# Kernel optimization log

Hardware: AMD Instinct MI355X
Metric: run time of the kernel (lower is better)

Reference implementation:

```python
import jax, jax.numpy as jnp
import numpy as np

EMBEDDING_DIM = 32  # hard-coded in the original module
HEAD_SIZE = 2048
B, T = 8, 2048  # T must be <= HEAD_SIZE (tril buffer is head_size x head_size)


def setup_inputs() -> dict:
    key = jax.random.key(0)
    kx, kk, kq, kv = jax.random.split(key, 4)
    x = jax.random.normal(kx, (B, T, EMBEDDING_DIM), dtype=jnp.float32)
    # torch nn.Linear(EMBEDDING_DIM, head_size, bias=False) computes x @ W.T with
    # W of shape [head_size, EMBEDDING_DIM]; we store the transposed [in, out] form.
    scale = (1.0 / np.sqrt(EMBEDDING_DIM)).astype(np.float32)
    Wk = jax.random.normal(kk, (EMBEDDING_DIM, HEAD_SIZE), dtype=jnp.float32) * scale
    Wq = jax.random.normal(kq, (EMBEDDING_DIM, HEAD_SIZE), dtype=jnp.float32) * scale
    Wv = jax.random.normal(kv, (EMBEDDING_DIM, HEAD_SIZE), dtype=jnp.float32) * scale
    return {"x": x, "Wk": Wk, "Wq": Wq, "Wv": Wv}


def reference(x, Wk, Wq, Wv):
    b, t, c = x.shape  # c == EMBEDDING_DIM
    k = x @ Wk  # [b, t, head_size]
    q = x @ Wq  # [b, t, head_size]
    v = x @ Wv  # [b, t, head_size]
    # NB: original scales by c**-0.5 where c is the *input* embedding dim (32).
    scores = jnp.einsum('bth,bsh->bts', q, k) * (c ** -0.5)  # [b, t, t]
    causal = jnp.tril(jnp.ones((t, t), dtype=bool))
    scores = jnp.where(causal, scores, -jnp.inf)
    attn = jax.nn.softmax(scores, axis=-1)
    return attn @ v  # [b, t, head_size]
```

## Files before the change

### kernel.cpp

```cpp
#include <hip/hip_runtime.h>

#define BB 8
#define TT 2048
#define CC 32
#define HH 2048
#define QB 128
#define HB 128
#define SCALE 0.17677669529663687f
#define K2E   0.25503255741f

typedef _Float16 f16;
typedef f16 f16x8 __attribute__((ext_vector_type(8)));
typedef f16 f16x4 __attribute__((ext_vector_type(4)));
typedef float f32x4 __attribute__((ext_vector_type(4)));

__global__ __launch_bounds__(256) void mk_kernel(const float* __restrict__ Wq,
                                                 const float* __restrict__ Wk,
                                                 float* __restrict__ M) {
    const int o = blockIdx.x * 4 + (threadIdx.x >> 6);
    const int lane = threadIdx.x & 63;
    const int c = o >> 5, cp = o & 31;
    const float4* a = (const float4*)(Wq + (size_t)c * HH);
    const float4* b = (const float4*)(Wk + (size_t)cp * HH);
    float acc = 0.f;
    #pragma unroll
    for (int i = 0; i < 8; i++) {
        float4 av = a[lane + i * 64], bv = b[lane + i * 64];
        acc += av.x * bv.x + av.y * bv.y + av.z * bv.z + av.w * bv.w;
    }
    #pragma unroll
    for (int off = 1; off < 64; off <<= 1) acc += __shfl_xor(acc, off, 64);
    if (lane == 0) M[c * 32 + cp] = acc;
}

__global__ __launch_bounds__(256) void proj2_kernel(const float* __restrict__ x,
                                                    const float* __restrict__ M,
                                                    f16* __restrict__ yh,
                                                    f16* __restrict__ xh) {
    __shared__ float xs2[32][33];
    const int tid = threadIdx.x;
    const size_t rbase = (size_t)blockIdx.x * 32;
    const int r = tid >> 3, c4 = (tid & 7) * 4;
    float4 xv = *(const float4*)&x[(rbase + r) * CC + c4];
    xs2[r][c4 + 0] = xv.x; xs2[r][c4 + 1] = xv.y;
    xs2[r][c4 + 2] = xv.z; xs2[r][c4 + 3] = xv.w;
    f16x4 xf = {(f16)xv.x, (f16)xv.y, (f16)xv.z, (f16)xv.w};
    *(f16x4*)&xh[(rbase + r) * CC + c4] = xf;
    __syncthreads();
    float a0 = 0.f, a1 = 0.f, a2 = 0.f, a3 = 0.f;
    #pragma unroll
    for (int c = 0; c < 32; c++) {
        const float xr = xs2[r][c];
        const float4 mv = *(const float4*)&M[c * 32 + c4];
        a0 += xr * mv.x; a1 += xr * mv.y; a2 += xr * mv.z; a3 += xr * mv.w;
    }
    f16x4 yf = {(f16)a0, (f16)a1, (f16)a2, (f16)a3};
    *(f16x4*)&yh[(rbase + r) * CC + c4] = yf;
}

__global__ __launch_bounds__(256, 3) void attn_kernel(
    const f16* __restrict__ xh, const f16* __restrict__ yh,
    const float* __restrict__ Wv, float* __restrict__ out)
{
    const int bid = blockIdx.x;
    const int qt  = 15 - (bid >> 7);
    const int b   = (bid >> 4) & 7;
    const int ht  = bid & 15;
    const int tid = threadIdx.x;
    const int lane = tid & 63, wave = tid >> 6;
    const int g = lane >> 4, li = lane & 15;
    const int wr = wave >> 1, wc = wave & 1;
    const int qbase = qt * QB, hbase = ht * HB;
    const int qrow0 = qbase + wr * 64;
    const int nst = 2 * qt + 2;

    __shared__ __align__(16) f16 smem[64 * 40 + 128 * 72 + 128 * 72];
    f16 (*xs)[40] = (f16(*)[40])smem;
    f16 (*vt)[72] = (f16(*)[72])(smem + 64 * 40);
    f16 (*ps)[72] = (f16(*)[72])(smem + 64 * 40 + 128 * 72);
    __shared__ float mh[2][128];
    __shared__ float lh[2][128];

    const f16* xp = xh + (size_t)b * TT * CC;
    const f16* yp = yh + (size_t)b * TT * CC;

    f16x8 af[4];
    #pragma unroll
    for (int rf = 0; rf < 4; rf++)
        af[rf] = *(const f16x8*)&yp[(size_t)(qbase + wr * 64 + rf * 16 + li) * CC + g * 8];

    f16x8 wv[4];
    #pragma unroll
    for (int hf = 0; hf < 4; hf++) {
        #pragma unroll
        for (int j = 0; j < 8; j++)
            wv[hf][j] = (f16)Wv[(size_t)(g * 8 + j) * HH + hbase + wc * 64 + hf * 16 + li];
    }

    const int rr = tid >> 2, c8 = (tid & 3) * 8;

    float mp[4] = {-3e38f, -3e38f, -3e38f, -3e38f};
    f16 (*x4)[64][40] = (f16(*)[64][40])smem;
    for (int ch = 0; ch * 4 < nst; ch++) {
        __syncthreads();
        #pragma unroll
        for (int j = 0; j < 4; j++) {
            const int st = ch * 4 + j;
            if (st < nst)
                *(f16x8*)&x4[j][rr][c8] = *(const f16x8*)&xp[(size_t)(st * 64 + rr) * CC + c8];
        }
        __syncthreads();
        #pragma unroll
        for (int j = 0; j < 4; j++) {
            const int st = ch * 4 + j;
            if (st < nst) {
                const int sbase = st * 64;
                const bool diag = (sbase + 63) > qrow0;
                #pragma unroll
                for (int sfi = 0; sfi < 2; sfi++) {
                    const f16x8 xa = *(const f16x8*)&x4[j][(2 * wc + sfi) * 16 + li][g * 8];
                    const int sb2 = sbase + (2 * wc + sfi) * 16 + g * 4;
                    #pragma unroll
                    for (int rf = 0; rf < 4; rf++) {
                        f32x4 z = {};
                        f32x4 sc = __builtin_amdgcn_mfma_f32_16x16x32_f16(xa, af[rf], z, 0, 0, 0);
                        const int qg = qbase + wr * 64 + rf * 16 + li;
                        #pragma unroll
                        for (int reg = 0; reg < 4; reg++) {
                            float v = sc[reg];
                            if (diag && (sb2 + reg) > qg) v = -3e38f;
                            mp[rf] = fmaxf(mp[rf], v);
                        }
                    }
                }
            }
        }
    }
    #pragma unroll
    for (int rf = 0; rf < 4; rf++) {
        mp[rf] = fmaxf(mp[rf], __shfl_xor(mp[rf], 16, 64));
        mp[rf] = fmaxf(mp[rf], __shfl_xor(mp[rf], 32, 64));
    }
    if (g == 0) {
        #pragma unroll
        for (int rf = 0; rf < 4; rf++) mh[wc][wr * 64 + rf * 16 + li] = mp[rf];
    }
    __syncthreads();
    float m2[4];
    #pragma unroll
    for (int rf = 0; rf < 4; rf++)
        m2[rf] = fmaxf(mh[0][wr * 64 + rf * 16 + li], mh[1][wr * 64 + rf * 16 + li]) * K2E;

    f16x8 xn = *(const f16x8*)&xp[(size_t)rr * CC + c8];
    *(f16x8*)&xs[rr][c8] = xn;
    __syncthreads();

    f32x4 o[4][4] = {};
    float lp[4] = {0.f, 0.f, 0.f, 0.f};
    f16x4 pf0[4], pf1[4];
    f16x4 vf0[4], vf1[4];

    for (int st = 0; st <= nst; st++) {
        const int sbase = st * 64;
        const bool haveQ = (st < nst);
        if (haveQ) {
            if (st + 1 < nst)
                xn = *(const f16x8*)&xp[(size_t)((st + 1) * 64 + rr) * CC + c8];
            const bool diag = (sbase + 63) > qrow0;
            const f16x8 xa0 = *(const f16x8*)&xs[(2 * wc + 0) * 16 + li][g * 8];
            const f16x8 xa1 = *(const f16x8*)&xs[(2 * wc + 1) * 16 + li][g * 8];
            const f16x8 xw0 = *(const f16x8*)&xs[(2 * wr + 0) * 16 + li][g * 8];
            const f16x8 xw1 = *(const f16x8*)&xs[(2 * wr + 1) * 16 + li][g * 8];
            #pragma unroll
            for (int sfi = 0; sfi < 2; sfi++) {
                const f16x8 xa = sfi ? xa1 : xa0;
                const int sb2 = sbase + (2 * wc + sfi) * 16 + g * 4;
                #pragma unroll
                for (int rf = 0; rf < 4; rf++) {
                    f32x4 z = {};
                    f32x4 sc = __builtin_amdgcn_mfma_f32_16x16x32_f16(xa, af[rf], z, 0, 0, 0);
                    const int qg = qbase + wr * 64 + rf * 16 + li;
                    f16x4 pv;
                    #pragma unroll
                    for (int reg = 0; reg < 4; reg++) {
                        float e = exp2f(fmaf(sc[reg], K2E, -m2[rf]));
                        if (diag && (sb2 + reg) > qg) e = 0.f;
                        lp[rf] += e;
                        pv[reg] = (f16)e;
                    }
                    if (sfi == 0) pf0[rf] = pv; else pf1[rf] = pv;
                }
            }
            #pragma unroll
            for (int sfw = 0; sfw < 2; sfw++) {
                const f16x8 xw = sfw ? xw1 : xw0;
                #pragma unroll
                for (int hf = 0; hf < 4; hf++) {
                    f32x4 z = {};
                    f32x4 vc = __builtin_amdgcn_mfma_f32_16x16x32_f16(xw, wv[hf], z, 0, 0, 0);
                    f16x4 vv4;
                    #pragma unroll
                    for (int reg = 0; reg < 4; reg++) vv4[reg] = (f16)vc[reg];
                    if (sfw == 0) vf0[hf] = vv4; else vf1[hf] = vv4;
                }
            }
        }
        if (st > 0) {
            #pragma unroll
            for (int kk = 0; kk < 2; kk++) {
                f16x8 pa[4];
                #pragma unroll
                for (int rf = 0; rf < 4; rf++) {
                    const int prow = wr * 64 + rf * 16 + li;
                    pa[rf] = *(const f16x8*)&ps[prow][(kk * 32 + g * 8) ^ (((prow >> 2) & 3) << 4)];
                }
                #pragma unroll
                for (int hf = 0; hf < 4; hf++) {
                    const int vrow = wc * 64 + hf * 16 + li;
                    const f16x8 vb = *(const f16x8*)&vt[vrow][(kk * 32 + g * 8) ^ (((vrow >> 3) & 3) << 4)];
                    #pragma unroll
                    for (int rf = 0; rf < 4; rf++)
                        o[rf][hf] = __builtin_amdgcn_mfma_f32_16x16x32_f16(pa[rf], vb, o[rf][hf], 0, 0, 0);
                }
            }
        }
        __syncthreads();
        if (haveQ) {
            #pragma unroll
            for (int rf = 0; rf < 4; rf++) {
                const int prow = wr * 64 + rf * 16 + li;
                const int swp = ((prow >> 2) & 3) << 4;
                *(f16x4*)&ps[prow][((2 * wc + 0) * 16 + g * 4) ^ swp] = pf0[rf];
                *(f16x4*)&ps[prow][((2 * wc + 1) * 16 + g * 4) ^ swp] = pf1[rf];
            }
            #pragma unroll
            for (int hf = 0; hf < 4; hf++) {
                const int vrow = wc * 64 + hf * 16 + li;
                const int swv = ((vrow >> 3) & 3) << 4;
                *(f16x4*)&vt[vrow][((2 * wr + 0) * 16 + g * 4) ^ swv] = vf0[hf];
                *(f16x4*)&vt[vrow][((2 * wr + 1) * 16 + g * 4) ^ swv] = vf1[hf];
            }
            if (st + 1 < nst)
                *(f16x8*)&xs[rr][c8] = xn;
            __syncthreads();
        }
    }

    #pragma unroll
    for (int rf = 0; rf < 4; rf++) {
        lp[rf] += __shfl_xor(lp[rf], 16, 64);
        lp[rf] += __shfl_xor(lp[rf], 32, 64);
    }
    if (g == 0) {
        #pragma unroll
        for (int rf = 0; rf < 4; rf++) lh[wc][wr * 64 + rf * 16 + li] = lp[rf];
    }
    __syncthreads();
    float* op = out + (size_t)b * TT * HH;
    #pragma unroll
    for (int rf = 0; rf < 4; rf++) {
        #pragma unroll
        for (int reg = 0; reg < 4; reg++) {
            const int ql = wr * 64 + rf * 16 + g * 4 + reg;
            const float inv = 1.f / (lh[0][ql] + lh[1][ql]);
            #pragma unroll
            for (int hf = 0; hf < 4; hf++)
                op[(size_t)(qbase + ql) * HH + hbase + wc * 64 + hf * 16 + li] = o[rf][hf][reg] * inv;
        }
    }
}

extern "C" void kernel_launch(void* const* d_in, const int* in_sizes, int n_in,
                              void* d_out, int out_size, void* d_ws, size_t ws_size,
                              hipStream_t stream) {
    const float* x  = (const float*)d_in[0];
    const float* Wk = (const float*)d_in[1];
    const float* Wq = (const float*)d_in[2];
    const float* Wv = (const float*)d_in[3];
    float* out = (float*)d_out;

    float* Mp = (float*)d_ws;
    f16* xh = (f16*)((char*)d_ws + 4096);
    f16* yh = xh + (size_t)BB * TT * CC;

    mk_kernel<<<256, 256, 0, stream>>>(Wq, Wk, Mp);
    proj2_kernel<<<(BB * TT) / 32, 256, 0, stream>>>(x, Mp, yh, xh);
    attn_kernel<<<BB * (TT / QB) * (HH / HB), 256, 0, stream>>>(xh, yh, Wv, out);
}
```

Baseline: 484.1 us.

## Precompute softmax row max and sum in a separate kernel shared across head tiles

The per-row softmax max and normalizer are now computed once per (batch, query tile) in a new ml_kernel and written to workspace. Before, each of the 16 head-tile blocks recomputed the max pass redundantly. The attention kernel now loads these stats instead of running its own max pass and sum accumulation. This removes duplicated QK score work, at the cost of an extra launch and a small serial kernel with only 128 blocks of uneven causal work.

```diff
diff --git a/kernel.cpp b/kernel.cpp
--- a/kernel.cpp
+++ b/kernel.cpp
@@ -6,7 +6,6 @@
 #define HH 2048
 #define QB 128
 #define HB 128
-#define SCALE 0.17677669529663687f
 #define K2E   0.25503255741f
 
 typedef _Float16 f16;
@@ -58,9 +57,142 @@
     *(f16x4*)&yh[(rbase + r) * CC + c4] = yf;
 }
 
+__global__ __launch_bounds__(256) void ml_kernel(const f16* __restrict__ xh,
+                                                 const f16* __restrict__ yh,
+                                                 float* __restrict__ m2g,
+                                                 float* __restrict__ lig) {
+    const int b = blockIdx.x >> 4, qt = blockIdx.x & 15;
+    const int tid = threadIdx.x;
+    const int lane = tid & 63, wave = tid >> 6;
+    const int g = lane >> 4, li = lane & 15;
+    const int wr = wave >> 1, wc = wave & 1;
+    const int qbase = qt * QB;
+    const int qrow0 = qbase + wr * 64;
+    const int nst = 2 * qt + 2;
+
+    __shared__ __align__(16) f16 x4[4][64][40];
+    __shared__ float mh[2][128];
+    __shared__ float lh[2][128];
+
+    const f16* xp = xh + (size_t)b * TT * CC;
+    const f16* yp = yh + (size_t)b * TT * CC;
+
+    f16x8 af[4];
+    #pragma unroll
+    for (int rf = 0; rf < 4; rf++)
+        af[rf] = *(const f16x8*)&yp[(size_t)(qbase + wr * 64 + rf * 16 + li) * CC + g * 8];
+
+    const int rr = tid >> 2, c8 = (tid & 3) * 8;
+
+    float mp[4] = {-3e38f, -3e38f, -3e38f, -3e38f};
+    for (int ch = 0; ch * 4 < nst; ch++) {
+        __syncthreads();
+        #pragma unroll
+        for (int j = 0; j < 4; j++) {
+            const int st = ch * 4 + j;
+            if (st < nst)
+                *(f16x8*)&x4[j][rr][c8] = *(const f16x8*)&xp[(size_t)(st * 64 + rr) * CC + c8];
+        }
+        __syncthreads();
+        #pragma unroll
+        for (int j = 0; j < 4; j++) {
+            const int st = ch * 4 + j;
+            if (st < nst) {
+                const int sbase = st * 64;
+                const bool diag = (sbase + 63) > qrow0;
+                #pragma unroll
+                for (int sfi = 0; sfi < 2; sfi++) {
+                    const f16x8 xa = *(const f16x8*)&x4[j][(2 * wc + sfi) * 16 + li][g * 8];
+                    const int sb2 = sbase + (2 * wc + sfi) * 16 + g * 4;
+                    #pragma unroll
+                    for (int rf = 0; rf < 4; rf++) {
+                        f32x4 z = {};
+                        f32x4 sc = __builtin_amdgcn_mfma_f32_16x16x32_f16(xa, af[rf], z, 0, 0, 0);
+                        const int qg = qbase + wr * 64 + rf * 16 + li;
+                        #pragma unroll
+                        for (int reg = 0; reg < 4; reg++) {
+                            float v = sc[reg];
+                            if (diag && (sb2 + reg) > qg) v = -3e38f;
+                            mp[rf] = fmaxf(mp[rf], v);
+                        }
+                    }
+                }
+            }
+        }
+    }
+    #pragma unroll
+    for (int rf = 0; rf < 4; rf++) {
+        mp[rf] = fmaxf(mp[rf], __shfl_xor(mp[rf], 16, 64));
+        mp[rf] = fmaxf(mp[rf], __shfl_xor(mp[rf], 32, 64));
+    }
+    if (g == 0) {
+        #pragma unroll
+        for (int rf = 0; rf < 4; rf++) mh[wc][wr * 64 + rf * 16 + li] = mp[rf];
+    }
+    __syncthreads();
+    float m2[4];
+    #pragma unroll
+    for (int rf = 0; rf < 4; rf++)
+        m2[rf] = fmaxf(mh[0][wr * 64 + rf * 16 + li], mh[1][wr * 64 + rf * 16 + li]) * K2E;
+
+    float lp[4] = {0.f, 0.f, 0.f, 0.f};
+    for (int ch = 0; ch * 4 < nst; ch++) {
+        __syncthreads();
+        #pragma unroll
+        for (int j = 0; j < 4; j++) {
+            const int st = ch * 4 + j;
+            if (st < nst)
+                *(f16x8*)&x4[j][rr][c8] = *(const f16x8*)&xp[(size_t)(st * 64 + rr) * CC + c8];
+        }
+        __syncthreads();
+        #pragma unroll
+        for (int j = 0; j < 4; j++) {
+            const int st = ch * 4 + j;
+            if (st < nst) {
+                const int sbase = st * 64;
+                const bool diag = (sbase + 63) > qrow0;
+                #pragma unroll
+                for (int sfi = 0; sfi < 2; sfi++) {
+                    const f16x8 xa = *(const f16x8*)&x4[j][(2 * wc + sfi) * 16 + li][g * 8];
+                    const int sb2 = sbase + (2 * wc + sfi) * 16 + g * 4;
+                    #pragma unroll
+                    for (int rf = 0; rf < 4; rf++) {
+                        f32x4 z = {};
+                        f32x4 sc = __builtin_amdgcn_mfma_f32_16x16x32_f16(xa, af[rf], z, 0, 0, 0);
+                        const int qg = qbase + wr * 64 + rf * 16 + li;
+                        #pragma unroll
+                        for (int reg = 0; reg < 4; reg++) {
+                            float e = exp2f(fmaf(sc[reg], K2E, -m2[rf]));
+                            if (diag && (sb2 + reg) > qg) e = 0.f;
+                            lp[rf] += e;
+                        }
+                    }
+                }
+            }
+        }
+    }
+    #pragma unroll
+    for (int rf = 0; rf < 4; rf++) {
+        lp[rf] += __shfl_xor(lp[rf], 16, 64);
+        lp[rf] += __shfl_xor(lp[rf], 32, 64);
+    }
+    if (g == 0) {
+        #pragma unroll
+        for (int rf = 0; rf < 4; rf++) lh[wc][wr * 64 + rf * 16 + li] = lp[rf];
+    }
+    __syncthreads();
+    if (tid < 128) {
+        const float mv = fmaxf(mh[0][tid], mh[1][tid]) * K2E;
+        const float lv = lh[0][tid] + lh[1][tid];
+        m2g[(size_t)b * TT + qbase + tid] = mv;
+        lig[(size_t)b * TT + qbase + tid] = 1.f / lv;
+    }
+}
+
 __global__ __launch_bounds__(256, 3) void attn_kernel(
     const f16* __restrict__ xh, const f16* __restrict__ yh,
-    const float* __restrict__ Wv, float* __restrict__ out)
+    const float* __restrict__ Wv, const float* __restrict__ m2g,
+    const float* __restrict__ lig, float* __restrict__ out)
 {
     const int bid = blockIdx.x;
     const int qt  = 15 - (bid >> 7);
@@ -78,12 +210,17 @@
     f16 (*xs)[40] = (f16(*)[40])smem;
     f16 (*vt)[72] = (f16(*)[72])(smem + 64 * 40);
     f16 (*ps)[72] = (f16(*)[72])(smem + 64 * 40 + 128 * 72);
-    __shared__ float mh[2][128];
-    __shared__ float lh[2][128];
+    __shared__ float mrow[128];
+    __shared__ float lrow[128];
 
     const f16* xp = xh + (size_t)b * TT * CC;
     const f16* yp = yh + (size_t)b * TT * CC;
 
+    if (tid < 128) {
+        mrow[tid] = m2g[(size_t)b * TT + qbase + tid];
+        lrow[tid] = lig[(size_t)b * TT + qbase + tid];
+    }
+
     f16x8 af[4];
     #pragma unroll
     for (int rf = 0; rf < 4; rf++)
@@ -98,65 +235,16 @@
     }
 
     const int rr = tid >> 2, c8 = (tid & 3) * 8;
-
-    float mp[4] = {-3e38f, -3e38f, -3e38f, -3e38f};
-    f16 (*x4)[64][40] = (f16(*)[64][40])smem;
-    for (int ch = 0; ch * 4 < nst; ch++) {
-        __syncthreads();
-        #pragma unroll
-        for (int j = 0; j < 4; j++) {
-            const int st = ch * 4 + j;
-            if (st < nst)
-                *(f16x8*)&x4[j][rr][c8] = *(const f16x8*)&xp[(size_t)(st * 64 + rr) * CC + c8];
-        }
-        __syncthreads();
-        #pragma unroll
-        for (int j = 0; j < 4; j++) {
-            const int st = ch * 4 + j;
-            if (st < nst) {
-                const int sbase = st * 64;
-                const bool diag = (sbase + 63) > qrow0;
-                #pragma unroll
-                for (int sfi = 0; sfi < 2; sfi++) {
-                    const f16x8 xa = *(const f16x8*)&x4[j][(2 * wc + sfi) * 16 + li][g * 8];
-                    const int sb2 = sbase + (2 * wc + sfi) * 16 + g * 4;
-                    #pragma unroll
-                    for (int rf = 0; rf < 4; rf++) {
-                        f32x4 z = {};
-                        f32x4 sc = __builtin_amdgcn_mfma_f32_16x16x32_f16(xa, af[rf], z, 0, 0, 0);
-                        const int qg = qbase + wr * 64 + rf * 16 + li;
-                        #pragma unroll
-                        for (int reg = 0; reg < 4; reg++) {
-                            float v = sc[reg];
-                            if (diag && (sb2 + reg) > qg) v = -3e38f;
-                            mp[rf] = fmaxf(mp[rf], v);
-                        }
-                    }
-                }
-            }
-        }
-    }
-    #pragma unroll
-    for (int rf = 0; rf < 4; rf++) {
-        mp[rf] = fmaxf(mp[rf], __shfl_xor(mp[rf], 16, 64));
-        mp[rf] = fmaxf(mp[rf], __shfl_xor(mp[rf], 32, 64));
-    }
-    if (g == 0) {
-        #pragma unroll
-        for (int rf = 0; rf < 4; rf++) mh[wc][wr * 64 + rf * 16 + li] = mp[rf];
-    }
-    __syncthreads();
-    float m2[4];
-    #pragma unroll
-    for (int rf = 0; rf < 4; rf++)
-        m2[rf] = fmaxf(mh[0][wr * 64 + rf * 16 + li], mh[1][wr * 64 + rf * 16 + li]) * K2E;
 
     f16x8 xn = *(const f16x8*)&xp[(size_t)rr * CC + c8];
     *(f16x8*)&xs[rr][c8] = xn;
     __syncthreads();
 
+    float m2[4];
+    #pragma unroll
+    for (int rf = 0; rf < 4; rf++) m2[rf] = mrow[wr * 64 + rf * 16 + li];
+
     f32x4 o[4][4] = {};
-    float lp[4] = {0.f, 0.f, 0.f, 0.f};
     f16x4 pf0[4], pf1[4];
     f16x4 vf0[4], vf1[4];
 
@@ -185,7 +273,6 @@
                     for (int reg = 0; reg < 4; reg++) {
                         float e = exp2f(fmaf(sc[reg], K2E, -m2[rf]));
                         if (diag && (sb2 + reg) > qg) e = 0.f;
-                        lp[rf] += e;
                         pv[reg] = (f16)e;
                     }
                     if (sfi == 0) pf0[rf] = pv; else pf1[rf] = pv;
@@ -246,23 +333,13 @@
         }
     }
 
-    #pragma unroll
-    for (int rf = 0; rf < 4; rf++) {
-        lp[rf] += __shfl_xor(lp[rf], 16, 64);
-        lp[rf] += __shfl_xor(lp[rf], 32, 64);
-    }
-    if (g == 0) {
-        #pragma unroll
-        for (int rf = 0; rf < 4; rf++) lh[wc][wr * 64 + rf * 16 + li] = lp[rf];
-    }
-    __syncthreads();
     float* op = out + (size_t)b * TT * HH;
     #pragma unroll
     for (int rf = 0; rf < 4; rf++) {
         #pragma unroll
         for (int reg = 0; reg < 4; reg++) {
             const int ql = wr * 64 + rf * 16 + g * 4 + reg;
-            const float inv = 1.f / (lh[0][ql] + lh[1][ql]);
+            const float inv = lrow[ql];
             #pragma unroll
             for (int hf = 0; hf < 4; hf++)
                 op[(size_t)(qbase + ql) * HH + hbase + wc * 64 + hf * 16 + li] = o[rf][hf][reg] * inv;
@@ -282,8 +359,11 @@
     float* Mp = (float*)d_ws;
     f16* xh = (f16*)((char*)d_ws + 4096);
     f16* yh = xh + (size_t)BB * TT * CC;
+    float* m2g = (float*)(yh + (size_t)BB * TT * CC);
+    float* lig = m2g + (size_t)BB * TT;
 
     mk_kernel<<<256, 256, 0, stream>>>(Wq, Wk, Mp);
     proj2_kernel<<<(BB * TT) / 32, 256, 0, stream>>>(x, Mp, yh, xh);
-    attn_kernel<<<BB * (TT / QB) * (HH / HB), 256, 0, stream>>>(xh, yh, Wv, out);
-}
+    ml_kernel<<<BB * (TT / QB), 256, 0, stream>>>(xh, yh, m2g, lig);
+    attn_kernel<<<BB * (TT / QB) * (HH / HB), 256, 0, stream>>>(xh, yh, Wv, m2g, lig, out);
+}
```

Result: faster. 432.4 us (-10.7%).
